# Optimization experiments

Measured on AMD Instinct MI355X. Metric: run time of the kernel, lower is better.

## Reference

```python
import jax, jax.numpy as jnp
import numpy as np

B, N, F = 1024, 784, 1
C1, C2, H, NCLS = 32, 32, 512, 10


def setup_inputs() -> dict:
    key = jax.random.key(0)
    ks = jax.random.split(key, 10)
    x = jax.random.normal(ks[0], (B, N, F), jnp.float32)
    # dense (renormalized-style) adjacency, shared across the batch; rows roughly sum to ~1
    a = jax.random.uniform(ks[1], (N, N), jnp.float32) * (2.0 / N)
    def glorot(k, shape):
        lim = np.sqrt(6.0 / (shape[0] + shape[1])).astype(np.float32)
        return jax.random.uniform(k, shape, jnp.float32, -lim, lim)
    return {
        "x": x,
        "a": a,
        "w1": glorot(ks[2], (F, C1)),
        "b1": jnp.zeros((C1,), jnp.float32),
        "w2": glorot(ks[3], (C1, C2)),
        "b2": jnp.zeros((C2,), jnp.float32),
        "wf1": glorot(ks[4], (N * C2, H)),
        "bf1": jnp.zeros((H,), jnp.float32),
        "wf2": glorot(ks[5], (H, NCLS)),
        "bf2": jnp.zeros((NCLS,), jnp.float32),
    }


def _graph_conv(x, a, w, b):
    # Spektral GraphConv (batch mode): elu(A @ (X @ W) + b)
    xw = jnp.einsum('bnf,fc->bnc', x, w)
    agg = jnp.einsum('nm,bmc->bnc', a, xw)
    return jax.nn.elu(agg + b)


def reference(x, a, w1, b1, w2, b2, wf1, bf1, wf2, bf2):
    h = _graph_conv(x, a, w1, b1)          # [B, N, 32]
    h = _graph_conv(h, a, w2, b2)          # [B, N, 32]
    h = h.reshape(h.shape[0], -1)          # Flatten -> [B, N*32]
    h = jax.nn.relu(h @ wf1 + bf1)         # [B, 512]
    return jax.nn.softmax(h @ wf2 + bf2, axis=-1)  # [B, 10]
```

## Files before the change

### kernel.cpp

```cpp
#include <hip/hip_runtime.h>
#include <hip/hip_bf16.h>
#include <math.h>

#define BATCH 1024
#define NREAL 784
#define NPAD  896
#define C1D   32
#define C2D   32
#define HDIM  512
#define NCLS  10
#define KFC   25088

#define KS_G1 7
#define KS_FC 14

#define BM 128
#define BN 128
#define BK 32

using bf16x8  = __attribute__((ext_vector_type(8))) __bf16;
using floatx4 = __attribute__((ext_vector_type(4))) float;

__device__ __forceinline__ float elu_f(float t) {
    return t > 0.f ? t : (__expf(t) - 1.f);
}

__device__ __forceinline__ void wg_barrier_lds() {
    asm volatile("s_waitcnt lgkmcnt(0)\n\ts_barrier" ::: "memory");
}

template<int MODE>
__launch_bounds__(256)
__global__ void gemm_bt(const __hip_bfloat16* __restrict__ A, int lda,
                        const __hip_bfloat16* __restrict__ Bm, int ldb,
                        int kIters, int kPerZ, size_t sliceStride,
                        float* __restrict__ outF, int ldc,
                        __hip_bfloat16* __restrict__ outH,
                        const float* __restrict__ bias)
{
    __shared__ __align__(16) __hip_bfloat16 As[2][BM * BK];
    __shared__ __align__(16) __hip_bfloat16 Bs[2][BN * BK];

    const int tid  = threadIdx.x;
    const int lane = tid & 63;
    const int wave = tid >> 6;
    const int wi = wave >> 1, wj = wave & 1;

    const int m0 = blockIdx.y * BM;
    const int n0 = blockIdx.x * BN;
    const int kBase = blockIdx.z * kPerZ;

    const int rowInChunk = lane >> 2;
    const int kOff8 = (lane & 3) * 8;

    const __hip_bfloat16* aSrc0 = A  + (size_t)(m0 + (wave * 2 + 0) * 16 + rowInChunk) * lda + kBase + kOff8;
    const __hip_bfloat16* aSrc1 = A  + (size_t)(m0 + (wave * 2 + 1) * 16 + rowInChunk) * lda + kBase + kOff8;
    const __hip_bfloat16* bSrc0 = Bm + (size_t)(n0 + (wave * 2 + 0) * 16 + rowInChunk) * ldb + kBase + kOff8;
    const __hip_bfloat16* bSrc1 = Bm + (size_t)(n0 + (wave * 2 + 1) * 16 + rowInChunk) * ldb + kBase + kOff8;

    const int wSlot = (((lane & 3) + ((lane >> 3) & 3)) & 3) * 8;
    const int ldsW0 = (wave * 2 + 0) * 512 + rowInChunk * 32 + wSlot;
    const int ldsW1 = ldsW0 + 512;

    const int rSlot = ((((lane >> 4) + (((lane & 15) >> 1) & 3)) & 3)) * 8;
    const int rRow  = lane & 15;

    floatx4 acc[4][4];
    const floatx4 zero4 = {0.f, 0.f, 0.f, 0.f};
    #pragma unroll
    for (int i = 0; i < 4; i++)
        #pragma unroll
        for (int j = 0; j < 4; j++) acc[i][j] = zero4;

    int4 aA0, aA1, bA0, bA1;
    int4 aB0, aB1, bB0, bB1;

    aA0 = *(const int4*)aSrc0; aA1 = *(const int4*)aSrc1;
    bA0 = *(const int4*)bSrc0; bA1 = *(const int4*)bSrc1;
    aSrc0 += BK; aSrc1 += BK; bSrc0 += BK; bSrc1 += BK;
    aB0 = *(const int4*)aSrc0; aB1 = *(const int4*)aSrc1;
    bB0 = *(const int4*)bSrc0; bB1 = *(const int4*)bSrc1;
    aSrc0 += BK; aSrc1 += BK; bSrc0 += BK; bSrc1 += BK;

    *(int4*)(&As[0][ldsW0]) = aA0;
    *(int4*)(&As[0][ldsW1]) = aA1;
    *(int4*)(&Bs[0][ldsW0]) = bA0;
    *(int4*)(&Bs[0][ldsW1]) = bA1;
    wg_barrier_lds();

    for (int kt = 0; kt < kIters; kt += 2) {
        const bool more = (kt + 2 < kIters);

        {
            bf16x8 af[4], bfr[4];
            #pragma unroll
            for (int mi = 0; mi < 4; mi++)
                af[mi] = *(const bf16x8*)(&As[0][(wi * 64 + mi * 16 + rRow) * BK + rSlot]);
            #pragma unroll
            for (int nj = 0; nj < 4; nj++)
                bfr[nj] = *(const bf16x8*)(&Bs[0][(wj * 64 + nj * 16 + rRow) * BK + rSlot]);

            if (more) {
                aA0 = *(const int4*)aSrc0; aA1 = *(const int4*)aSrc1;
                bA0 = *(const int4*)bSrc0; bA1 = *(const int4*)bSrc1;
                aSrc0 += BK; aSrc1 += BK; bSrc0 += BK; bSrc1 += BK;
            }
            *(int4*)(&As[1][ldsW0]) = aB0;
            *(int4*)(&As[1][ldsW1]) = aB1;
            *(int4*)(&Bs[1][ldsW0]) = bB0;
            *(int4*)(&Bs[1][ldsW1]) = bB1;

            #pragma unroll
            for (int mi = 0; mi < 4; mi++)
                #pragma unroll
                for (int nj = 0; nj < 4; nj++)
                    acc[mi][nj] = __builtin_amdgcn_mfma_f32_16x16x32_bf16(af[mi], bfr[nj], acc[mi][nj], 0, 0, 0);

            wg_barrier_lds();
        }

        {
            bf16x8 af[4], bfr[4];
            #pragma unroll
            for (int mi = 0; mi < 4; mi++)
                af[mi] = *(const bf16x8*)(&As[1][(wi * 64 + mi * 16 + rRow) * BK + rSlot]);
            #pragma unroll
            for (int nj = 0; nj < 4; nj++)
                bfr[nj] = *(const bf16x8*)(&Bs[1][(wj * 64 + nj * 16 + rRow) * BK + rSlot]);

            if (more) {
                aB0 = *(const int4*)aSrc0; aB1 = *(const int4*)aSrc1;
                bB0 = *(const int4*)bSrc0; bB1 = *(const int4*)bSrc1;
                aSrc0 += BK; aSrc1 += BK; bSrc0 += BK; bSrc1 += BK;
                *(int4*)(&As[0][ldsW0]) = aA0;
                *(int4*)(&As[0][ldsW1]) = aA1;
                *(int4*)(&Bs[0][ldsW0]) = bA0;
                *(int4*)(&Bs[0][ldsW1]) = bA1;
            }

            #pragma unroll
            for (int mi = 0; mi < 4; mi++)
                #pragma unroll
                for (int nj = 0; nj < 4; nj++)
                    acc[mi][nj] = __builtin_amdgcn_mfma_f32_16x16x32_bf16(af[mi], bfr[nj], acc[mi][nj], 0, 0, 0);

            wg_barrier_lds();
        }
    }

    #pragma unroll
    for (int mi = 0; mi < 4; mi++) {
        #pragma unroll
        for (int nj = 0; nj < 4; nj++) {
            #pragma unroll
            for (int r = 0; r < 4; r++) {
                const int row = m0 + wi * 64 + mi * 16 + (lane >> 4) * 4 + r;
                const int col = n0 + wj * 64 + nj * 16 + (lane & 15);
                const float v = acc[mi][nj][r];
                if (MODE == 1) {
                    if (row < NREAL) {
                        const int c = col & 31, b = col >> 5;
                        const float t = elu_f(v + bias[c]);
                        outH[(size_t)b * KFC + row * 32 + c] = __float2bfloat16(t);
                    }
                } else {
                    outF[(size_t)blockIdx.z * sliceStride + (size_t)row * ldc + col] = v;
                }
            }
        }
    }
}

__global__ void convX(const float* __restrict__ x, __hip_bfloat16* __restrict__ Xbf) {
    const int idx = blockIdx.x * 256 + threadIdx.x;
    if (idx >= BATCH * NPAD) return;
    const int m = idx % NPAD, b = idx / NPAD;
    const float v = (m < NREAL) ? x[(size_t)b * NREAL + m] : 0.f;
    Xbf[idx] = __float2bfloat16(v);
}

__global__ void convA(const float* __restrict__ a, __hip_bfloat16* __restrict__ Abf) {
    const int idx = blockIdx.x * 256 + threadIdx.x;
    if (idx >= NPAD * NPAD) return;
    const int m = idx % NPAD, n = idx / NPAD;
    const float v = (m < NREAL && n < NREAL) ? a[(size_t)n * NREAL + m] : 0.f;
    Abf[idx] = __float2bfloat16(v);
}

__global__ void convW(const float* __restrict__ wf1, __hip_bfloat16* __restrict__ Wt) {
    __shared__ float tile[32][33];
    const int k0 = blockIdx.x * 32, h0 = blockIdx.y * 32;
    const int tx = threadIdx.x, ty = threadIdx.y;
    #pragma unroll
    for (int i = 0; i < 4; i++)
        tile[ty * 4 + i][tx] = wf1[(size_t)(k0 + ty * 4 + i) * HDIM + h0 + tx];
    __syncthreads();
    #pragma unroll
    for (int i = 0; i < 4; i++)
        Wt[(size_t)(h0 + ty * 4 + i) * KFC + k0 + tx] = __float2bfloat16(tile[tx][ty * 4 + i]);
}

__global__ void layer1_fuse(const float* __restrict__ Ypart,
                            const float* __restrict__ w1, const float* __restrict__ b1,
                            const float* __restrict__ w2,
                            __hip_bfloat16* __restrict__ Tt)
{
    __shared__ __align__(16) float sW2[C1D * C2D];
    __shared__ float sw1[C1D], sb1[C1D];
    const int tid = threadIdx.x;
    for (int i = tid; i < C1D * C2D; i += 128) sW2[i] = w2[i];
    if (tid < C1D) { sw1[tid] = w1[tid]; sb1[tid] = b1[tid]; }
    __syncthreads();

    const int m = blockIdx.x * 128 + tid;
    const int b = blockIdx.y;
    float y = 0.f;
    #pragma unroll
    for (int z = 0; z < KS_G1; z++)
        y += Ypart[(size_t)z * (BATCH * NPAD) + (size_t)b * NPAD + m];

    float h[C1D];
    #pragma unroll
    for (int c1 = 0; c1 < C1D; c1++) h[c1] = elu_f(y * sw1[c1] + sb1[c1]);

    float4 t4[8];
    #pragma unroll
    for (int q = 0; q < 8; q++) t4[q] = make_float4(0.f, 0.f, 0.f, 0.f);
    #pragma unroll
    for (int c1 = 0; c1 < C1D; c1++) {
        const float hv = h[c1];
        const float4* row = (const float4*)(sW2 + c1 * C2D);
        #pragma unroll
        for (int q = 0; q < 8; q++) {
            const float4 w = row[q];
            t4[q].x += hv * w.x; t4[q].y += hv * w.y;
            t4[q].z += hv * w.z; t4[q].w += hv * w.w;
        }
    }
    const float* tf = (const float*)t4;
    #pragma unroll
    for (int c = 0; c < C2D; c++)
        Tt[((size_t)(b * 32 + c)) * NPAD + m] = __float2bfloat16(tf[c]);
}

__global__ void fc2_softmax(const float* __restrict__ part, const float* __restrict__ bf1,
                            const float* __restrict__ wf2, const float* __restrict__ bf2,
                            float* __restrict__ out)
{
    __shared__ float sW[HDIM * NCLS];
    __shared__ float sb[NCLS];
    const int tid = threadIdx.x;
    for (int i = tid; i < HDIM * NCLS; i += 256) sW[i] = wf2[i];
    if (tid < NCLS) sb[tid] = bf2[tid];
    __syncthreads();

    const int lane = tid & 63, wave = tid >> 6;
    const int b = blockIdx.x * 4 + wave;

    float acc[NCLS];
    #pragma unroll
    for (int c = 0; c < NCLS; c++) acc[c] = 0.f;
    #pragma unroll
    for (int q = 0; q < 8; q++) {
        const int h = q * 64 + lane;
        float hv = bf1[h];
        #pragma unroll
        for (int z = 0; z < KS_FC; z++)
            hv += part[(size_t)z * (BATCH * HDIM) + (size_t)b * HDIM + h];
        hv = hv > 0.f ? hv : 0.f;
        #pragma unroll
        for (int c = 0; c < NCLS; c++) acc[c] += hv * sW[h * NCLS + c];
    }
    #pragma unroll
    for (int c = 0; c < NCLS; c++) {
        #pragma unroll
        for (int off = 32; off >= 1; off >>= 1) acc[c] += __shfl_down(acc[c], off);
    }
    if (lane == 0) {
        float mx = -1e30f;
        #pragma unroll
        for (int c = 0; c < NCLS; c++) { acc[c] += sb[c]; mx = fmaxf(mx, acc[c]); }
        float e[NCLS], s = 0.f;
        #pragma unroll
        for (int c = 0; c < NCLS; c++) { e[c] = __expf(acc[c] - mx); s += e[c]; }
        const float inv = 1.f / s;
        #pragma unroll
        for (int c = 0; c < NCLS; c++) out[(size_t)b * NCLS + c] = e[c] * inv;
    }
}

extern "C" void kernel_launch(void* const* d_in, const int* in_sizes, int n_in,
                              void* d_out, int out_size, void* d_ws, size_t ws_size,
                              hipStream_t stream)
{
    const float* x   = (const float*)d_in[0];
    const float* a   = (const float*)d_in[1];
    const float* w1  = (const float*)d_in[2];
    const float* b1  = (const float*)d_in[3];
    const float* w2  = (const float*)d_in[4];
    const float* b2  = (const float*)d_in[5];
    const float* wf1 = (const float*)d_in[6];
    const float* bf1 = (const float*)d_in[7];
    const float* wf2 = (const float*)d_in[8];
    const float* bf2 = (const float*)d_in[9];
    float* out = (float*)d_out;

    char* ws = (char*)d_ws;
    __hip_bfloat16* h2f  = (__hip_bfloat16*)(ws + 0);
    float*          Ypart= (float*)(ws + 0);
    __hip_bfloat16* Tt   = (__hip_bfloat16*)(ws + 51380224);
    __hip_bfloat16* Wt   = (__hip_bfloat16*)(ws + 51380224);
    float*          part = (float*)(ws + 77070336);
    __hip_bfloat16* Abf  = (__hip_bfloat16*)(ws + 110100480);
    __hip_bfloat16* Xbf  = (__hip_bfloat16*)(ws + 111706112);

    convX<<<(BATCH * NPAD + 255) / 256, 256, 0, stream>>>(x, Xbf);
    convA<<<(NPAD * NPAD + 255) / 256, 256, 0, stream>>>(a, Abf);

    gemm_bt<2><<<dim3(NPAD / BN, BATCH / BM, KS_G1), 256, 0, stream>>>(
        Xbf, NPAD, Abf, NPAD, (NPAD / KS_G1) / BK, NPAD / KS_G1,
        (size_t)BATCH * NPAD, Ypart, NPAD, nullptr, nullptr);

    layer1_fuse<<<dim3(NPAD / 128, BATCH), 128, 0, stream>>>(Ypart, w1, b1, w2, Tt);

    gemm_bt<1><<<dim3((BATCH * 32) / BN, NPAD / BM, 1), 256, 0, stream>>>(
        Abf, NPAD, Tt, NPAD, NPAD / BK, 0, 0, nullptr, 0, h2f, b2);

    convW<<<dim3(KFC / 32, HDIM / 32), dim3(32, 8), 0, stream>>>(wf1, Wt);

    gemm_bt<2><<<dim3(HDIM / BN, BATCH / BM, KS_FC), 256, 0, stream>>>(
        h2f, KFC, Wt, KFC, (KFC / KS_FC) / BK, KFC / KS_FC,
        (size_t)BATCH * HDIM, part, HDIM, nullptr, nullptr);

    fc2_softmax<<<BATCH / 4, 256, 0, stream>>>(part, bf1, wf2, bf2, out);
}
```

Baseline: 306.6 us.

## Replace second graph-conv GEMM with 256x256 direct-to-LDS pipelined kernel

Swaps the 128x128 tiled GEMM for the A·T aggregation with a new 512-thread kernel using 256x256 tiles and a K-step of 64. It loads tiles straight from global memory into LDS through global_load_lds, with a swizzled layout to avoid bank conflicts. It also interleaves the next-tile loads with MFMA phases and raises wave priority around the MFMAs. The goal is higher MFMA utilization and less register-staged global traffic, at the cost of more LDS and registers and a grid padded to 1024 rows, with clamped row reads.

```diff
diff --git a/kernel.cpp b/kernel.cpp
--- a/kernel.cpp
+++ b/kernel.cpp
@@ -27,6 +27,21 @@
 
 __device__ __forceinline__ void wg_barrier_lds() {
     asm volatile("s_waitcnt lgkmcnt(0)\n\ts_barrier" ::: "memory");
+}
+
+__device__ __forceinline__ void bar() {
+    asm volatile("s_barrier" ::: "memory");
+}
+
+__device__ __forceinline__ void lgkm0_fence() {
+    asm volatile("s_waitcnt lgkmcnt(0)" ::: "memory");
+    __builtin_amdgcn_sched_barrier(0);
+}
+
+__device__ __forceinline__ void gload_lds16(const __hip_bfloat16* g, __hip_bfloat16* l) {
+    __builtin_amdgcn_global_load_lds(
+        (const __attribute__((address_space(1))) void*)g,
+        (__attribute__((address_space(3))) void*)l, 16, 0, 0);
 }
 
 template<int MODE>
@@ -165,6 +180,143 @@
                     }
                 } else {
                     outF[(size_t)blockIdx.z * sliceStride + (size_t)row * ldc + col] = v;
+                }
+            }
+        }
+    }
+}
+
+#define KT_G3 14
+
+#define G3_PHASE(MH, NH, PRE_BAR, ISS_A, ISS_B)                                   \
+  {                                                                               \
+    bf16x8 a0_[4], a1_[4], b0_[2], b1_[2];                                        \
+    _Pragma("unroll")                                                             \
+    for (int i_ = 0; i_ < 4; i_++) {                                              \
+      const int ro_ = aRowOff + ((MH) * 4 + i_) * 1024;                           \
+      a0_[i_] = *(const bf16x8*)(&As[cur][ro_ + koff0]);                          \
+      a1_[i_] = *(const bf16x8*)(&As[cur][ro_ + koff1]);                          \
+    }                                                                             \
+    _Pragma("unroll")                                                             \
+    for (int j_ = 0; j_ < 2; j_++) {                                              \
+      const int ro_ = bRowOff + ((NH) * 2 + j_) * 1024;                           \
+      b0_[j_] = *(const bf16x8*)(&Bs[cur][ro_ + koff0]);                          \
+      b1_[j_] = *(const bf16x8*)(&Bs[cur][ro_ + koff1]);                          \
+    }                                                                             \
+    if (ISS_A) {                                                                  \
+      _Pragma("unroll")                                                           \
+      for (int j_ = 0; j_ < 4; j_++)                                              \
+        gload_lds16(aSrc[j_] + kNext, &As[nb][(w4 + j_) * 512]);                  \
+    }                                                                             \
+    if (ISS_B) {                                                                  \
+      _Pragma("unroll")                                                           \
+      for (int j_ = 0; j_ < 4; j_++)                                              \
+        gload_lds16(bSrc[j_] + kNext, &Bs[nb][(w4 + j_) * 512]);                  \
+    }                                                                             \
+    if (PRE_BAR) bar();                                                           \
+    lgkm0_fence();                                                                \
+    __builtin_amdgcn_s_setprio(1);                                                \
+    _Pragma("unroll")                                                             \
+    for (int j_ = 0; j_ < 2; j_++)                                                \
+      _Pragma("unroll")                                                           \
+      for (int i_ = 0; i_ < 4; i_++)                                              \
+        acc[(MH) * 4 + i_][(NH) * 2 + j_] = __builtin_amdgcn_mfma_f32_16x16x32_bf16( \
+            a0_[i_], b0_[j_], acc[(MH) * 4 + i_][(NH) * 2 + j_], 0, 0, 0);        \
+    _Pragma("unroll")                                                             \
+    for (int j_ = 0; j_ < 2; j_++)                                                \
+      _Pragma("unroll")                                                           \
+      for (int i_ = 0; i_ < 4; i_++)                                              \
+        acc[(MH) * 4 + i_][(NH) * 2 + j_] = __builtin_amdgcn_mfma_f32_16x16x32_bf16( \
+            a1_[i_], b1_[j_], acc[(MH) * 4 + i_][(NH) * 2 + j_], 0, 0, 0);        \
+    __builtin_amdgcn_s_setprio(0);                                                \
+    bar();                                                                        \
+  }
+
+__launch_bounds__(512)
+__global__ void gemm256_g3(const __hip_bfloat16* __restrict__ Ag,
+                           const __hip_bfloat16* __restrict__ Bg,
+                           __hip_bfloat16* __restrict__ outH,
+                           const float* __restrict__ bias)
+{
+    __shared__ __align__(16) __hip_bfloat16 As[2][256 * 64];
+    __shared__ __align__(16) __hip_bfloat16 Bs[2][256 * 64];
+
+    const int tid  = threadIdx.x;
+    const int lane = tid & 63;
+    const int wave = tid >> 6;
+    const int WM = wave >> 2, WN = wave & 3;
+    const int w4 = wave * 4;
+
+    const int mR = blockIdx.y * 256;
+    const int nR = blockIdx.x * 256;
+
+    const int rRow = lane & 15;
+    const int gHi  = lane >> 4;
+    const int rot  = lane & 7;
+    const int koff0 = (((gHi + rot) & 7) << 3);
+    const int koff1 = ((((4 + gHi) + rot) & 7) << 3);
+    const int aRowOff = (WM * 128 + rRow) * 64;
+    const int bRowOff = (WN * 64 + rRow) * 64;
+
+    const int rowLoc = lane >> 3;
+    const int gOff   = ((((lane & 7) - rowLoc) & 7) << 3);
+    const __hip_bfloat16* aSrc[4];
+    const __hip_bfloat16* bSrc[4];
+    #pragma unroll
+    for (int j = 0; j < 4; j++) {
+        int ra = mR + (w4 + j) * 8 + rowLoc;
+        if (ra > NPAD - 1) ra = NPAD - 1;
+        aSrc[j] = Ag + (size_t)ra * NPAD + gOff;
+        const int rb = nR + (w4 + j) * 8 + rowLoc;
+        bSrc[j] = Bg + (size_t)rb * NPAD + gOff;
+    }
+
+    floatx4 acc[8][4];
+    const floatx4 zero4 = {0.f, 0.f, 0.f, 0.f};
+    #pragma unroll
+    for (int i = 0; i < 8; i++)
+        #pragma unroll
+        for (int j = 0; j < 4; j++) acc[i][j] = zero4;
+
+    #pragma unroll
+    for (int j = 0; j < 4; j++) gload_lds16(aSrc[j],      &As[0][(w4 + j) * 512]);
+    #pragma unroll
+    for (int j = 0; j < 4; j++) gload_lds16(bSrc[j],      &Bs[0][(w4 + j) * 512]);
+    #pragma unroll
+    for (int j = 0; j < 4; j++) gload_lds16(aSrc[j] + 64, &As[1][(w4 + j) * 512]);
+    #pragma unroll
+    for (int j = 0; j < 4; j++) gload_lds16(bSrc[j] + 64, &Bs[1][(w4 + j) * 512]);
+    asm volatile("s_waitcnt vmcnt(8)" ::: "memory");
+    bar();
+
+    for (int t = 0; t < KT_G3; ++t) {
+        const int cur = t & 1;
+        const int nb  = cur ^ 1;
+        const int kNext = (t + 1) * 64;
+        const bool iss = (t >= 1) & (t < KT_G3 - 1);
+
+        if (t) {
+            asm volatile("s_waitcnt vmcnt(0)" ::: "memory");
+            bar();
+        }
+        G3_PHASE(0, 0, false, iss, false)
+        G3_PHASE(0, 1, true,  false, iss)
+        G3_PHASE(1, 0, true,  false, false)
+        G3_PHASE(1, 1, true,  false, false)
+    }
+
+    #pragma unroll
+    for (int mi = 0; mi < 8; mi++) {
+        #pragma unroll
+        for (int nj = 0; nj < 4; nj++) {
+            #pragma unroll
+            for (int r = 0; r < 4; r++) {
+                const int row = mR + WM * 128 + mi * 16 + gHi * 4 + r;
+                const int col = nR + WN * 64 + nj * 16 + rRow;
+                if (row < NREAL) {
+                    const int c = col & 31, b = col >> 5;
+                    const float v = elu_f(acc[mi][nj][r] + bias[c]);
+                    outH[(size_t)b * KFC + row * 32 + c] = __float2bfloat16(v);
                 }
             }
         }
@@ -323,8 +475,7 @@
 
     layer1_fuse<<<dim3(NPAD / 128, BATCH), 128, 0, stream>>>(Ypart, w1, b1, w2, Tt);
 
-    gemm_bt<1><<<dim3((BATCH * 32) / BN, NPAD / BM, 1), 256, 0, stream>>>(
-        Abf, NPAD, Tt, NPAD, NPAD / BK, 0, 0, nullptr, 0, h2f, b2);
+    gemm256_g3<<<dim3(BATCH * 32 / 256, 1024 / 256), 512, 0, stream>>>(Abf, Tt, h2f, b2);
 
     convW<<<dim3(KFC / 32, HDIM / 32), dim3(32, 8), 0, stream>>>(wf1, Wt);
 
```

Result: no change. 311.5 us (+1.6%).

## Replace layer-2 aggregation GEMM with 256x256 tile kernel using direct-to-LDS loads

Applied to the files above, without the earlier changes.

Swaps the generic 128x128 gemm_bt for the A@T layer-2 aggregation for a new 512-thread kernel with 256x256 output tiles. It uses global_load_lds to stream 64-wide K slices straight into a 4-stage, XOR-swizzled LDS ring, with split-phase barriers and s_setprio around the MFMA bursts. The aim is more data reuse per tile and better overlap of loads with the 16x16x32 MFMAs. In exchange, register pressure rises, and the M dimension is padded to 1024 with clamped row reads, which adds wasted compute on rows beyond 784.

```diff
diff --git a/kernel.cpp b/kernel.cpp
--- a/kernel.cpp
+++ b/kernel.cpp
@@ -27,6 +27,21 @@
 
 __device__ __forceinline__ void wg_barrier_lds() {
     asm volatile("s_waitcnt lgkmcnt(0)\n\ts_barrier" ::: "memory");
+}
+
+__device__ __forceinline__ void bar() {
+    asm volatile("s_barrier" ::: "memory");
+}
+
+__device__ __forceinline__ void lgkm0_fence() {
+    asm volatile("s_waitcnt lgkmcnt(0)" ::: "memory");
+    __builtin_amdgcn_sched_barrier(0);
+}
+
+__device__ __forceinline__ void gload_lds16(const __hip_bfloat16* g, __hip_bfloat16* l) {
+    __builtin_amdgcn_global_load_lds(
+        (const __attribute__((address_space(1))) void*)g,
+        (__attribute__((address_space(3))) void*)l, 16, 0, 0);
 }
 
 template<int MODE>
@@ -165,6 +180,153 @@
                     }
                 } else {
                     outF[(size_t)blockIdx.z * sliceStride + (size_t)row * ldc + col] = v;
+                }
+            }
+        }
+    }
+}
+
+#define KT_G3 14
+
+#define STAGE_A(tt, hh) do {                                                    \
+    const int s_ = (2 * (tt) + (hh)) & 3;                                       \
+    gload_lds16(aSrcH[hh][0] + (tt) * 64, &Ah[s_][(wave * 2 + 0) * 512]);       \
+    gload_lds16(aSrcH[hh][1] + (tt) * 64, &Ah[s_][(wave * 2 + 1) * 512]);       \
+} while (0)
+
+#define STAGE_B(tt, hh) do {                                                    \
+    const int s_ = (2 * (tt) + (hh)) & 3;                                       \
+    gload_lds16(bSrcH[hh][0] + (tt) * 64, &Bh[s_][(wave * 2 + 0) * 512]);       \
+    gload_lds16(bSrcH[hh][1] + (tt) * 64, &Bh[s_][(wave * 2 + 1) * 512]);       \
+} while (0)
+
+#define G3_PHASE(QM, QN, ISS)                                                   \
+  {                                                                             \
+    const int sA_ = (2 * t + (QM)) & 3;                                         \
+    const int sB_ = (2 * t + (QN)) & 3;                                         \
+    bf16x8 a0_[4], a1_[4], b0_[2], b1_[2];                                      \
+    _Pragma("unroll")                                                           \
+    for (int mi_ = 0; mi_ < 4; mi_++) {                                         \
+      const int ro_ = aBase + mi_ * 1024;                                       \
+      a0_[mi_] = *(const bf16x8*)(&Ah[sA_][ro_ + koff0]);                       \
+      a1_[mi_] = *(const bf16x8*)(&Ah[sA_][ro_ + koff1]);                       \
+    }                                                                           \
+    _Pragma("unroll")                                                           \
+    for (int nj_ = 0; nj_ < 2; nj_++) {                                         \
+      const int ro_ = bBase + nj_ * 1024;                                       \
+      b0_[nj_] = *(const bf16x8*)(&Bh[sB_][ro_ + koff0]);                       \
+      b1_[nj_] = *(const bf16x8*)(&Bh[sB_][ro_ + koff1]);                       \
+    }                                                                           \
+    ISS                                                                         \
+    lgkm0_fence();                                                              \
+    __builtin_amdgcn_s_setprio(1);                                              \
+    _Pragma("unroll")                                                           \
+    for (int nj_ = 0; nj_ < 2; nj_++)                                           \
+      _Pragma("unroll")                                                         \
+      for (int mi_ = 0; mi_ < 4; mi_++)                                         \
+        acc[(QM) * 2 + (QN)][mi_][nj_] = __builtin_amdgcn_mfma_f32_16x16x32_bf16( \
+            a0_[mi_], b0_[nj_], acc[(QM) * 2 + (QN)][mi_][nj_], 0, 0, 0);       \
+    _Pragma("unroll")                                                           \
+    for (int nj_ = 0; nj_ < 2; nj_++)                                           \
+      _Pragma("unroll")                                                         \
+      for (int mi_ = 0; mi_ < 4; mi_++)                                         \
+        acc[(QM) * 2 + (QN)][mi_][nj_] = __builtin_amdgcn_mfma_f32_16x16x32_bf16( \
+            a1_[mi_], b1_[nj_], acc[(QM) * 2 + (QN)][mi_][nj_], 0, 0, 0);       \
+    __builtin_amdgcn_s_setprio(0);                                              \
+  }
+
+__launch_bounds__(512, 2)
+__global__ void gemm256_g3(const __hip_bfloat16* __restrict__ Ag,
+                           const __hip_bfloat16* __restrict__ Bg,
+                           __hip_bfloat16* __restrict__ outH,
+                           const float* __restrict__ bias)
+{
+    __shared__ __align__(16) __hip_bfloat16 Ah[4][128 * 64];
+    __shared__ __align__(16) __hip_bfloat16 Bh[4][128 * 64];
+
+    const int tid  = threadIdx.x;
+    const int lane = tid & 63;
+    const int wave = tid >> 6;
+    const int vm = wave >> 2, vn = wave & 3;
+
+    const int mR = blockIdx.y * 256;
+    const int nR = blockIdx.x * 256;
+
+    const int rRow = lane & 15;
+    const int gHi  = lane >> 4;
+    const int rot  = lane & 7;
+    const int koff0 = (((gHi + rot) & 7) << 3);
+    const int koff1 = ((((4 + gHi) + rot) & 7) << 3);
+    const int aBase = (vm * 64 + rRow) * 64;
+    const int bBase = (vn * 32 + rRow) * 64;
+
+    const int rowLoc = lane >> 3;
+    const int gOff   = ((((lane & 7) - rowLoc) & 7) << 3);
+    const __hip_bfloat16* aSrcH[2][2];
+    const __hip_bfloat16* bSrcH[2][2];
+    #pragma unroll
+    for (int h = 0; h < 2; h++)
+        #pragma unroll
+        for (int j = 0; j < 2; j++) {
+            int ra = mR + h * 128 + (wave * 2 + j) * 8 + rowLoc;
+            if (ra > NPAD - 1) ra = NPAD - 1;
+            aSrcH[h][j] = Ag + (size_t)ra * NPAD + gOff;
+            const int rb = nR + h * 128 + (wave * 2 + j) * 8 + rowLoc;
+            bSrcH[h][j] = Bg + (size_t)rb * NPAD + gOff;
+        }
+
+    const float bias0 = bias[rRow];
+    const float bias1 = bias[16 + rRow];
+
+    floatx4 acc[4][4][2];
+    const floatx4 zero4 = {0.f, 0.f, 0.f, 0.f};
+    #pragma unroll
+    for (int q = 0; q < 4; q++)
+        #pragma unroll
+        for (int i = 0; i < 4; i++)
+            #pragma unroll
+            for (int j = 0; j < 2; j++) acc[q][i][j] = zero4;
+
+    STAGE_A(0, 0);
+    STAGE_A(0, 1); STAGE_B(0, 1); STAGE_B(0, 0);
+    STAGE_A(1, 0);
+
+    #pragma unroll 2
+    for (int t = 0; t < KT_G3; ++t) {
+        if (t == KT_G3 - 1) { asm volatile("s_waitcnt vmcnt(0)" ::: "memory"); }
+        else                { asm volatile("s_waitcnt vmcnt(2)" ::: "memory"); }
+        bar();
+
+        G3_PHASE(0, 0, {
+            if (t + 1 < KT_G3) { STAGE_A(t + 1, 1); STAGE_B(t + 1, 1); STAGE_B(t + 1, 0); }
+        })
+        G3_PHASE(0, 1, { })
+
+        bar();
+
+        G3_PHASE(1, 0, {
+            if (t + 2 < KT_G3) { STAGE_A(t + 2, 0); }
+        })
+        G3_PHASE(1, 1, { })
+    }
+
+    #pragma unroll
+    for (int q = 0; q < 4; q++) {
+        const int qm = q >> 1, qn = q & 1;
+        #pragma unroll
+        for (int mi = 0; mi < 4; mi++) {
+            #pragma unroll
+            for (int nj = 0; nj < 2; nj++) {
+                #pragma unroll
+                for (int r = 0; r < 4; r++) {
+                    const int row = mR + qm * 128 + vm * 64 + mi * 16 + gHi * 4 + r;
+                    if (row < NREAL) {
+                        const int col = nR + qn * 128 + vn * 32 + nj * 16 + rRow;
+                        const int c = col & 31, b = col >> 5;
+                        const float bv = nj ? bias1 : bias0;
+                        const float v = elu_f(acc[q][mi][nj][r] + bv);
+                        outH[(size_t)b * KFC + row * 32 + c] = __float2bfloat16(v);
+                    }
                 }
             }
         }
@@ -323,8 +485,7 @@
 
     layer1_fuse<<<dim3(NPAD / 128, BATCH), 128, 0, stream>>>(Ypart, w1, b1, w2, Tt);
 
-    gemm_bt<1><<<dim3((BATCH * 32) / BN, NPAD / BM, 1), 256, 0, stream>>>(
-        Abf, NPAD, Tt, NPAD, NPAD / BK, 0, 0, nullptr, 0, h2f, b2);
+    gemm256_g3<<<dim3(BATCH * 32 / 256, 1024 / 256), 512, 0, stream>>>(Abf, Tt, h2f, b2);
 
     convW<<<dim3(KFC / 32, HDIM / 32), dim3(32, 8), 0, stream>>>(wf1, Wt);
 
```

Result: faster. 280.1 us (-8.6%).
